# Optimization experiments

Measured on AMD Instinct MI355X. Metric: run time of the kernel, lower is better.

Reference implementation:

```python
import jax, jax.numpy as jnp
import numpy as np

N_NODES = 50000
N_EDGES = 600000
N_RELS = 19
D_IN = 128
D_HID = 64
D_OUT = 2


def setup_inputs() -> dict:
    key = jax.random.key(0)
    ks = jax.random.split(key, 10)
    feat = jax.random.normal(ks[0], (N_NODES, D_IN), dtype=jnp.float32)
    src = jax.random.randint(ks[1], (N_EDGES,), 0, N_NODES)
    dst = jax.random.randint(ks[2], (N_EDGES,), 0, N_NODES)
    etype = jax.random.randint(ks[3], (N_EDGES,), 0, N_RELS)
    s1 = 1.0 / np.sqrt(D_IN)
    s2 = 1.0 / np.sqrt(D_HID)
    W1 = jax.random.normal(ks[4], (N_RELS, D_IN, D_HID), dtype=jnp.float32) * s1
    loop1 = jax.random.normal(ks[5], (D_IN, D_HID), dtype=jnp.float32) * s1
    b1 = jnp.zeros((D_HID,), dtype=jnp.float32)
    W2 = jax.random.normal(ks[6], (N_RELS, D_HID, D_OUT), dtype=jnp.float32) * s2
    loop2 = jax.random.normal(ks[7], (D_HID, D_OUT), dtype=jnp.float32) * s2
    b2 = jnp.zeros((D_OUT,), dtype=jnp.float32)
    return {"feat": feat, "W1": W1, "loop1": loop1, "b1": b1,
            "W2": W2, "loop2": loop2, "b2": b2,
            "src": src, "dst": dst, "etype": etype}


def _rel_graph_conv(h, W, loop_w, bias, src, dst, etype, activation):
    # Per-relation transform of all nodes: [N, R, O]; then gather per edge.
    # (num_rels * out_feat is small, so this is cheaper than gathering W per edge.)
    transformed = jnp.einsum('nd,rdo->nro', h, W)
    msg = transformed[src, etype]                      # [E, O] edge messages
    agg = jax.ops.segment_sum(msg, dst, num_segments=h.shape[0])  # scatter-add
    out = agg + h @ loop_w + bias                      # self-loop + bias
    if activation is not None:
        out = activation(out)
    return out


def reference(feat, W1, loop1, b1, W2, loop2, b2, src, dst, etype):
    h = _rel_graph_conv(feat, W1, loop1, b1, src, dst, etype, jax.nn.relu)
    h = _rel_graph_conv(h, W2, loop2, b2, src, dst, etype, None)
    return h
```

## Files before the change

### kernel.cpp

```cpp
#include <hip/hip_runtime.h>

#define N_NODES 50000
#define N_EDGES 600000
#define N_RELS  19
#define D_IN    128
#define D_HID   64
#define D_OUT   2

typedef unsigned short u16;
typedef unsigned int   u32;
typedef __attribute__((ext_vector_type(8))) short sfrag;
typedef __attribute__((ext_vector_type(4))) float f32x4;

__device__ __forceinline__ u16 f2bf(float f){
  union { float f; u32 i; } v; v.f = f;
  u32 r = v.i + 0x7fffu + ((v.i >> 16) & 1u);
  return (u16)(r >> 16);
}
__device__ __forceinline__ float bf2f(u16 u){
  union { u32 i; float f; } v; v.i = ((u32)u) << 16; return v.f;
}

__global__ void k_prep(const float* __restrict__ W1, const float* __restrict__ loop1,
                       const float* __restrict__ W2,
                       u16* __restrict__ W1Tb, u16* __restrict__ loop1Tb,
                       u16* __restrict__ W2Tb, int* __restrict__ hist_rel,
                       int* __restrict__ hist_dst){
  int idx = blockIdx.x * 256 + threadIdx.x;
  if (idx < N_RELS)  hist_rel[idx] = 0;
  if (idx < N_NODES) hist_dst[idx] = 0;
  const int T1 = N_RELS * D_HID * D_IN;
  const int T2 = T1 + N_RELS * 16 * D_HID;
  const int T3 = T2 + D_HID * D_IN;
  if (idx < T1) {
    int r = idx / (D_HID * D_IN);
    int t = idx - r * (D_HID * D_IN);
    int j = t >> 7, d = t & 127;
    W1Tb[idx] = f2bf(W1[(r * D_IN + d) * D_HID + j]);
  } else if (idx < T2) {
    int k2 = idx - T1;
    int r = k2 / (16 * D_HID);
    int t = k2 - r * (16 * D_HID);
    int n = t >> 6, k = t & 63;
    W2Tb[k2] = (n < D_OUT) ? f2bf(W2[(r * D_HID + k) * D_OUT + n]) : (u16)0;
  } else if (idx < T3) {
    int k2 = idx - T2;
    int j = k2 >> 7, d = k2 & 127;
    loop1Tb[k2] = f2bf(loop1[d * D_HID + j]);
  }
}

__global__ __launch_bounds__(256) void k_fused_pre(const float* __restrict__ feat,
                                                   u16* __restrict__ featb,
                                                   const int* __restrict__ et,
                                                   const int* __restrict__ dst,
                                                   int* __restrict__ hist_rel,
                                                   int* __restrict__ hist_dst){
  int i = blockIdx.x * 256 + threadIdx.x;
  float2 f = ((const float2*)feat)[i];
  ((u32*)featb)[i] = (u32)f2bf(f.x) | ((u32)f2bf(f.y) << 16);
  if (blockIdx.x < (N_EDGES + 255) / 256) {
    __shared__ int lh[N_RELS];
    int tid = threadIdx.x;
    if (tid < N_RELS) lh[tid] = 0;
    __syncthreads();
    int e = blockIdx.x * 256 + tid;
    if (e < N_EDGES) {
      atomicAdd(&lh[et[e]], 1);
      atomicAdd(&hist_dst[dst[e]], 1);
    }
    __syncthreads();
    if (tid < N_RELS && lh[tid]) atomicAdd(&hist_rel[tid], lh[tid]);
  }
}

__global__ void k_scan_rel(const int* __restrict__ hist, int* __restrict__ offs,
                           int* __restrict__ toff, int* __restrict__ cursor){
  if (threadIdx.x == 0) {
    int acc = 0, tacc = 0;
    offs[0] = 0; toff[0] = 0;
    for (int r = 0; r < N_RELS; ++r) {
      cursor[r] = acc;
      int c = hist[r];
      acc += c;                offs[r + 1] = acc;
      tacc += (c + 127) >> 7;  toff[r + 1] = tacc;
    }
  }
}

__global__ __launch_bounds__(256) void k_scan_dst1(const int* __restrict__ hist,
                                                   int* __restrict__ dcsr,
                                                   int* __restrict__ bsum){
  __shared__ int ws[4];
  int tid = threadIdx.x, lane = tid & 63, w = tid >> 6;
  int i = blockIdx.x * 256 + tid;
  int v = (i < N_NODES) ? hist[i] : 0;
  int x = v;
  #pragma unroll
  for (int o = 1; o < 64; o <<= 1) { int u = __shfl_up(x, o); if (lane >= o) x += u; }
  if (lane == 63) ws[w] = x;
  __syncthreads();
  int add = 0;
  for (int j = 0; j < w; ++j) add += ws[j];
  int excl = x - v + add;
  if (i < N_NODES) dcsr[i] = excl;
  if (tid == 255) bsum[blockIdx.x] = excl + v;
}

__global__ __launch_bounds__(256) void k_scan_dst2(int* __restrict__ bsum,
                                                   int* __restrict__ boff){
  __shared__ int ws[4];
  int tid = threadIdx.x, lane = tid & 63, w = tid >> 6;
  int v = (tid < 196) ? bsum[tid] : 0;
  int x = v;
  #pragma unroll
  for (int o = 1; o < 64; o <<= 1) { int u = __shfl_up(x, o); if (lane >= o) x += u; }
  if (lane == 63) ws[w] = x;
  __syncthreads();
  int add = 0;
  for (int j = 0; j < w; ++j) add += ws[j];
  if (tid < 196) boff[tid] = x - v + add;
}

__global__ __launch_bounds__(256) void k_scan_dst3(const int* __restrict__ boff,
                                                   int* __restrict__ dcsr,
                                                   int* __restrict__ cursor){
  int i = blockIdx.x * 256 + threadIdx.x;
  if (i < N_NODES) {
    int val = dcsr[i] + boff[blockIdx.x];
    dcsr[i] = val;
    cursor[i] = val;
  }
  if (i == 0) dcsr[N_NODES] = N_EDGES;
}

__global__ __launch_bounds__(256) void k_scatter_rel(const int* __restrict__ et,
                                                     int* __restrict__ cursor,
                                                     int* __restrict__ perm){
  __shared__ int lh[N_RELS], base[N_RELS];
  int tid = threadIdx.x;
  if (tid < N_RELS) lh[tid] = 0;
  __syncthreads();
  int e = blockIdx.x * 256 + tid;
  int r = 0, my = 0;
  bool valid = e < N_EDGES;
  if (valid) { r = et[e]; my = atomicAdd(&lh[r], 1); }
  __syncthreads();
  if (tid < N_RELS && lh[tid]) base[tid] = atomicAdd(&cursor[tid], lh[tid]);
  __syncthreads();
  if (valid) perm[base[r] + my] = e;
}

__global__ __launch_bounds__(256) void k_selfloop1_mfma(
    const u16* __restrict__ featb, const u16* __restrict__ loop1Tb,
    const float* __restrict__ b1, float* __restrict__ agg1f){
  __shared__ __align__(16) u16 Als[64][136];
  __shared__ __align__(16) u16 Bls[64][136];
  int tid = threadIdx.x;
  int base = blockIdx.x * 64;
  { int j = tid >> 2, seg = tid & 3;
    const uint4* g = (const uint4*)(loop1Tb + j * 128) + seg * 4;
    uint4* d = (uint4*)&Bls[j][seg * 32];
    d[0] = g[0]; d[1] = g[1]; d[2] = g[2]; d[3] = g[3]; }
  { int i = tid >> 2, seg = tid & 3;
    int n = base + i; if (n >= N_NODES) n = N_NODES - 1;
    const uint4* g = (const uint4*)(featb + (size_t)n * D_IN) + seg * 4;
    uint4* d = (uint4*)&Als[i][seg * 32];
    d[0] = g[0]; d[1] = g[1]; d[2] = g[2]; d[3] = g[3]; }
  __syncthreads();

  int w = tid >> 6, lane = tid & 63;
  int r16 = lane & 15, c4 = lane >> 4;
  sfrag aF[4];
  #pragma unroll
  for (int kk = 0; kk < 4; ++kk)
    aF[kk] = *(const sfrag*)&Als[w * 16 + r16][kk * 32 + c4 * 8];
  #pragma unroll
  for (int ct = 0; ct < 4; ++ct) {
    f32x4 acc = {0.f, 0.f, 0.f, 0.f};
    #pragma unroll
    for (int kk = 0; kk < 4; ++kk) {
      sfrag bF = *(const sfrag*)&Bls[ct * 16 + r16][kk * 32 + c4 * 8];
      acc = __builtin_amdgcn_mfma_f32_16x16x32_bf16(aF[kk], bF, acc, 0, 0, 0);
    }
    int col = ct * 16 + r16;
    float bias = b1[col];
    #pragma unroll
    for (int reg = 0; reg < 4; ++reg) {
      int row = base + w * 16 + c4 * 4 + reg;
      if (row < N_NODES) agg1f[(size_t)row * D_HID + col] = acc[reg] + bias;
    }
  }
}

__global__ __launch_bounds__(256) void k_edge1_mfma(
    const u16* __restrict__ featb, const u16* __restrict__ W1Tb,
    const int* __restrict__ src, const int* __restrict__ dst,
    const int* __restrict__ perm, const int* __restrict__ offs,
    const int* __restrict__ toff, const int* __restrict__ dcsr,
    int* __restrict__ cursor, u16* __restrict__ msgbuf){
  __shared__ __align__(16) u16 Als[128][136];
  __shared__ __align__(16) u16 Bls[64][136];
  __shared__ int posIds[128];
  int tid = threadIdx.x, lane = tid & 63, w = tid >> 6;

  int b = blockIdx.x;
  unsigned long long mm = __ballot((lane < N_RELS) && (b >= toff[lane + 1]));
  int rel = __popcll(mm);
  if (rel >= N_RELS) return;
  int ts = offs[rel] + ((b - toff[rel]) << 7);
  int vc = offs[rel + 1] - ts; if (vc > 128) vc = 128;

  {
    int j = tid >> 2, seg = tid & 3;
    const uint4* g = (const uint4*)(W1Tb + ((size_t)rel * 64 + j) * 128) + seg * 4;
    uint4* d = (uint4*)&Bls[j][seg * 32];
    d[0] = g[0]; d[1] = g[1]; d[2] = g[2]; d[3] = g[3];
  }
  #pragma unroll
  for (int p = 0; p < 2; ++p) {
    int i = p * 64 + (tid >> 2), seg = tid & 3;
    if (i < vc) {
      int e = perm[ts + i];
      if (seg == 0) posIds[i] = atomicAdd(&cursor[dst[e]], 1);
      const uint4* g = (const uint4*)(featb + (size_t)src[e] * D_IN) + seg * 4;
      uint4* d = (uint4*)&Als[i][seg * 32];
      d[0] = g[0]; d[1] = g[1]; d[2] = g[2]; d[3] = g[3];
    } else if (seg == 0) posIds[i] = -1;
  }
  __syncthreads();

  int r16 = lane & 15, c4 = lane >> 4;
  sfrag aF[2][4];
  #pragma unroll
  for (int mt = 0; mt < 2; ++mt)
    #pragma unroll
    for (int kk = 0; kk < 4; ++kk)
      aF[mt][kk] = *(const sfrag*)&Als[w * 32 + mt * 16 + r16][kk * 32 + c4 * 8];
  f32x4 accAll[2][4];
  #pragma unroll
  for (int ct = 0; ct < 4; ++ct) {
    sfrag bF[4];
    #pragma unroll
    for (int kk = 0; kk < 4; ++kk)
      bF[kk] = *(const sfrag*)&Bls[ct * 16 + r16][kk * 32 + c4 * 8];
    #pragma unroll
    for (int mt = 0; mt < 2; ++mt) {
      f32x4 acc = {0.f, 0.f, 0.f, 0.f};
      #pragma unroll
      for (int kk = 0; kk < 4; ++kk)
        acc = __builtin_amdgcn_mfma_f32_16x16x32_bf16(aF[mt][kk], bF[kk], acc, 0, 0, 0);
      accAll[mt][ct] = acc;
    }
  }
  float* msg = (float*)&Als[0][0];
  #pragma unroll
  for (int mt = 0; mt < 2; ++mt)
    #pragma unroll
    for (int ct = 0; ct < 4; ++ct) {
      int col = ct * 16 + r16;
      #pragma unroll
      for (int reg = 0; reg < 4; ++reg) {
        int row = w * 32 + mt * 16 + c4 * 4 + reg;
        msg[row * 68 + col] = accAll[mt][ct][reg];
      }
    }
  __syncthreads();
  { int row = tid >> 1, half = tid & 1;
    int pos = posIds[row];
    if (pos >= 0) {
      const float* mr = msg + row * 68 + half * 32;
      u32 pk[16];
      #pragma unroll
      for (int q = 0; q < 16; ++q)
        pk[q] = (u32)f2bf(mr[2 * q]) | ((u32)f2bf(mr[2 * q + 1]) << 16);
      uint4* d = (uint4*)(msgbuf + (size_t)pos * D_HID + half * 32);
      d[0] = *(uint4*)&pk[0];  d[1] = *(uint4*)&pk[4];
      d[2] = *(uint4*)&pk[8];  d[3] = *(uint4*)&pk[12];
    } }
}

__global__ __launch_bounds__(256) void k_agg_relu_self2(
    const u16* __restrict__ msgbuf, const int* __restrict__ dcsr,
    const float* __restrict__ agg1f, const float* __restrict__ loop2,
    const float* __restrict__ b2, u16* __restrict__ h1b,
    float* __restrict__ out){
  int wv = threadIdx.x >> 6, lane = threadIdx.x & 63;
  int n = blockIdx.x * 4 + wv;
  int s = dcsr[n], epos = dcsr[n + 1];
  int h = lane >> 5, c = lane & 31;
  float a0 = 0.f, a1 = 0.f;
  for (int i = s + h; i < epos; i += 2) {
    u32 v = ((const u32*)msgbuf)[(size_t)i * 32 + c];
    a0 += bf2f((u16)(v & 0xffffu));
    a1 += bf2f((u16)(v >> 16));
  }
  a0 += __shfl_down(a0, 32);
  a1 += __shfl_down(a1, 32);
  float p0 = 0.f, p1 = 0.f;
  if (h == 0) {
    float2 sl = ((const float2*)(agg1f + (size_t)n * D_HID))[c];
    float v0 = a0 + sl.x, v1 = a1 + sl.y;
    v0 = v0 > 0.f ? v0 : 0.f;
    v1 = v1 > 0.f ? v1 : 0.f;
    ((u32*)h1b)[(size_t)n * 32 + c] = (u32)f2bf(v0) | ((u32)f2bf(v1) << 16);
    float2 w0 = ((const float2*)loop2)[2 * c];
    float2 w1 = ((const float2*)loop2)[2 * c + 1];
    p0 = v0 * w0.x + v1 * w1.x;
    p1 = v0 * w0.y + v1 * w1.y;
  }
  #pragma unroll
  for (int off = 16; off; off >>= 1) {
    p0 += __shfl_down(p0, off);
    p1 += __shfl_down(p1, off);
  }
  if (lane == 0) {
    out[n * 2]     = p0 + b2[0];
    out[n * 2 + 1] = p1 + b2[1];
  }
}

__global__ __launch_bounds__(256) void k_edge2_mfma(
    const u16* __restrict__ h1b, const u16* __restrict__ W2Tb,
    const int* __restrict__ src, const int* __restrict__ dst,
    const int* __restrict__ perm, const int* __restrict__ offs,
    const int* __restrict__ toff, float* __restrict__ out){
  __shared__ __align__(16) u16 Als[128][72];
  __shared__ __align__(16) u16 Bls[16][72];
  __shared__ int dstIds[128];
  int tid = threadIdx.x, lane = tid & 63, w = tid >> 6;

  int b = blockIdx.x;
  unsigned long long mm = __ballot((lane < N_RELS) && (b >= toff[lane + 1]));
  int rel = __popcll(mm);
  if (rel >= N_RELS) return;
  int ts = offs[rel] + ((b - toff[rel]) << 7);
  int vc = offs[rel + 1] - ts; if (vc > 128) vc = 128;

  if (tid < 128) {
    ((uint4*)&Bls[tid >> 3][0])[tid & 7] = ((const uint4*)(W2Tb + (size_t)rel * 16 * 64))[tid];
  }
  {
    int i = tid >> 1, half = tid & 1;
    if (i < vc) {
      int e = perm[ts + i];
      if (half == 0) dstIds[i] = dst[e];
      const uint4* g = (const uint4*)(h1b + (size_t)src[e] * D_HID) + half * 4;
      uint4* d = (uint4*)&Als[i][half * 32];
      d[0] = g[0]; d[1] = g[1]; d[2] = g[2]; d[3] = g[3];
    } else if (half == 0) dstIds[i] = -1;
  }
  __syncthreads();

  int r16 = lane & 15, c4 = lane >> 4;
  #pragma unroll
  for (int mt = 0; mt < 2; ++mt) {
    f32x4 acc = {0.f, 0.f, 0.f, 0.f};
    #pragma unroll
    for (int kk = 0; kk < 2; ++kk) {
      sfrag aF = *(const sfrag*)&Als[w * 32 + mt * 16 + r16][kk * 32 + c4 * 8];
      sfrag bF = *(const sfrag*)&Bls[r16][kk * 32 + c4 * 8];
      acc = __builtin_amdgcn_mfma_f32_16x16x32_bf16(aF, bF, acc, 0, 0, 0);
    }
    if (r16 < D_OUT) {
      #pragma unroll
      for (int reg = 0; reg < 4; ++reg) {
        int row = w * 32 + mt * 16 + c4 * 4 + reg;
        int dn = dstIds[row];
        if (dn >= 0) atomicAdd(&out[dn * D_OUT + r16], acc[reg]);
      }
    }
  }
}

extern "C" void kernel_launch(void* const* d_in, const int* in_sizes, int n_in,
                              void* d_out, int out_size, void* d_ws, size_t ws_size,
                              hipStream_t stream){
  const float* feat  = (const float*)d_in[0];
  const float* W1    = (const float*)d_in[1];
  const float* loop1 = (const float*)d_in[2];
  const float* b1    = (const float*)d_in[3];
  const float* W2    = (const float*)d_in[4];
  const float* loop2 = (const float*)d_in[5];
  const float* b2    = (const float*)d_in[6];
  const int* src     = (const int*)d_in[7];
  const int* dst     = (const int*)d_in[8];
  const int* et      = (const int*)d_in[9];
  float* out = (float*)d_out;

  char* w = (char*)d_ws;
  u16*   W1Tb     = (u16*)(w);
  u16*   W2Tb     = (u16*)(w + 311296);
  u16*   loop1Tb  = (u16*)(w + 350208);
  int*   hist_rel = (int*)(w + 366592);
  int*   offs     = (int*)(w + 366720);
  int*   toff     = (int*)(w + 366848);
  int*   cur_rel  = (int*)(w + 366976);
  int*   bsum     = (int*)(w + 367104);
  int*   boff     = (int*)(w + 368128);
  int*   hist_dst = (int*)(w + 369152);
  int*   dcsr     = (int*)(w + 569152);
  int*   cur_dst  = (int*)(w + 769168);
  int*   perm     = (int*)(w + 969168);
  u16*   featb    = (u16*)(w + 3369168);
  float* agg1f    = (float*)(w + 16169168);
  u16*   h1b      = (u16*)(w + 28969168);
  u16*   msgbuf   = (u16*)(w + 35369168);

  const int MAX_TILES = (N_EDGES + 127) / 128 + N_RELS;

  k_prep          <<<716,   256, 0, stream>>>(W1, loop1, W2, W1Tb, loop1Tb, W2Tb,
                                              hist_rel, hist_dst);
  k_fused_pre     <<<12500, 256, 0, stream>>>(feat, featb, et, dst, hist_rel, hist_dst);
  k_scan_rel      <<<1,      64, 0, stream>>>(hist_rel, offs, toff, cur_rel);
  k_scan_dst1     <<<196,   256, 0, stream>>>(hist_dst, dcsr, bsum);
  k_scan_dst2     <<<1,     256, 0, stream>>>(bsum, boff);
  k_scan_dst3     <<<196,   256, 0, stream>>>(boff, dcsr, cur_dst);
  k_scatter_rel   <<<2344,  256, 0, stream>>>(et, cur_rel, perm);
  k_selfloop1_mfma<<<(N_NODES + 63) / 64, 256, 0, stream>>>(featb, loop1Tb, b1, agg1f);
  k_edge1_mfma    <<<MAX_TILES, 256, 0, stream>>>(featb, W1Tb, src, dst, perm, offs, toff,
                                                  dcsr, cur_dst, msgbuf);
  k_agg_relu_self2<<<12500, 256, 0, stream>>>(msgbuf, dcsr, agg1f, loop2, b2, h1b, out);
  k_edge2_mfma    <<<MAX_TILES, 256, 0, stream>>>(h1b, W2Tb, src, dst, perm, offs, toff, out);
}
```

Measured before the change: 329.5 us.

## Replace three-pass dst scan with atomic allocation and fuse self-loop into edge kernel

```diff
diff --git a/kernel.cpp b/kernel.cpp
--- a/kernel.cpp
+++ b/kernel.cpp
@@ -6,6 +6,8 @@
 #define D_IN    128
 #define D_HID   64
 #define D_OUT   2
+#define EDGE_TILES ((N_EDGES + 127) / 128 + N_RELS)
+#define SL_BLOCKS  ((N_NODES + 63) / 64)
 
 typedef unsigned short u16;
 typedef unsigned int   u32;
@@ -25,10 +27,11 @@
                        const float* __restrict__ W2,
                        u16* __restrict__ W1Tb, u16* __restrict__ loop1Tb,
                        u16* __restrict__ W2Tb, int* __restrict__ hist_rel,
-                       int* __restrict__ hist_dst){
+                       int* __restrict__ hist_dst, int* __restrict__ gcnt){
   int idx = blockIdx.x * 256 + threadIdx.x;
   if (idx < N_RELS)  hist_rel[idx] = 0;
   if (idx < N_NODES) hist_dst[idx] = 0;
+  if (idx == 0) gcnt[0] = 0;
   const int T1 = N_RELS * D_HID * D_IN;
   const int T2 = T1 + N_RELS * 16 * D_HID;
   const int T3 = T2 + D_HID * D_IN;
@@ -74,64 +77,35 @@
   }
 }
 
-__global__ void k_scan_rel(const int* __restrict__ hist, int* __restrict__ offs,
-                           int* __restrict__ toff, int* __restrict__ cursor){
-  if (threadIdx.x == 0) {
-    int acc = 0, tacc = 0;
-    offs[0] = 0; toff[0] = 0;
-    for (int r = 0; r < N_RELS; ++r) {
-      cursor[r] = acc;
-      int c = hist[r];
-      acc += c;                offs[r + 1] = acc;
-      tacc += (c + 127) >> 7;  toff[r + 1] = tacc;
-    }
-  }
-}
-
-__global__ __launch_bounds__(256) void k_scan_dst1(const int* __restrict__ hist,
-                                                   int* __restrict__ dcsr,
-                                                   int* __restrict__ bsum){
-  __shared__ int ws[4];
-  int tid = threadIdx.x, lane = tid & 63, w = tid >> 6;
-  int i = blockIdx.x * 256 + tid;
-  int v = (i < N_NODES) ? hist[i] : 0;
+__global__ __launch_bounds__(256) void k_alloc_scan(
+    const int* __restrict__ hist_dst, int* __restrict__ dstart,
+    int* __restrict__ cur_dst, int* __restrict__ gcnt,
+    const int* __restrict__ hist_rel, int* __restrict__ offs,
+    int* __restrict__ toff, int* __restrict__ cur_rel){
+  if (blockIdx.x == 196) {
+    if (threadIdx.x == 0) {
+      int acc = 0, tacc = 0;
+      offs[0] = 0; toff[0] = 0;
+      for (int r = 0; r < N_RELS; ++r) {
+        cur_rel[r] = acc;
+        int c = hist_rel[r];
+        acc += c;                offs[r + 1] = acc;
+        tacc += (c + 127) >> 7;  toff[r + 1] = tacc;
+      }
+    }
+    return;
+  }
+  __shared__ int wbase[4];
+  int tid = threadIdx.x, lane = tid & 63, wv = tid >> 6;
+  int n = blockIdx.x * 256 + tid;
+  int v = (n < N_NODES) ? hist_dst[n] : 0;
   int x = v;
   #pragma unroll
   for (int o = 1; o < 64; o <<= 1) { int u = __shfl_up(x, o); if (lane >= o) x += u; }
-  if (lane == 63) ws[w] = x;
-  __syncthreads();
-  int add = 0;
-  for (int j = 0; j < w; ++j) add += ws[j];
-  int excl = x - v + add;
-  if (i < N_NODES) dcsr[i] = excl;
-  if (tid == 255) bsum[blockIdx.x] = excl + v;
-}
-
-__global__ __launch_bounds__(256) void k_scan_dst2(int* __restrict__ bsum,
-                                                   int* __restrict__ boff){
-  __shared__ int ws[4];
-  int tid = threadIdx.x, lane = tid & 63, w = tid >> 6;
-  int v = (tid < 196) ? bsum[tid] : 0;
-  int x = v;
-  #pragma unroll
-  for (int o = 1; o < 64; o <<= 1) { int u = __shfl_up(x, o); if (lane >= o) x += u; }
-  if (lane == 63) ws[w] = x;
-  __syncthreads();
-  int add = 0;
-  for (int j = 0; j < w; ++j) add += ws[j];
-  if (tid < 196) boff[tid] = x - v + add;
-}
-
-__global__ __launch_bounds__(256) void k_scan_dst3(const int* __restrict__ boff,
-                                                   int* __restrict__ dcsr,
-                                                   int* __restrict__ cursor){
-  int i = blockIdx.x * 256 + threadIdx.x;
-  if (i < N_NODES) {
-    int val = dcsr[i] + boff[blockIdx.x];
-    dcsr[i] = val;
-    cursor[i] = val;
-  }
-  if (i == 0) dcsr[N_NODES] = N_EDGES;
+  if (lane == 63) wbase[wv] = atomicAdd(gcnt, x);
+  __syncthreads();
+  int start = wbase[wv] + x - v;
+  if (n < N_NODES) { dstart[n] = start; cur_dst[n] = start; }
 }
 
 __global__ __launch_bounds__(256) void k_scatter_rel(const int* __restrict__ et,
@@ -151,58 +125,48 @@
   if (valid) perm[base[r] + my] = e;
 }
 
-__global__ __launch_bounds__(256) void k_selfloop1_mfma(
-    const u16* __restrict__ featb, const u16* __restrict__ loop1Tb,
-    const float* __restrict__ b1, float* __restrict__ agg1f){
-  __shared__ __align__(16) u16 Als[64][136];
-  __shared__ __align__(16) u16 Bls[64][136];
-  int tid = threadIdx.x;
-  int base = blockIdx.x * 64;
-  { int j = tid >> 2, seg = tid & 3;
-    const uint4* g = (const uint4*)(loop1Tb + j * 128) + seg * 4;
-    uint4* d = (uint4*)&Bls[j][seg * 32];
-    d[0] = g[0]; d[1] = g[1]; d[2] = g[2]; d[3] = g[3]; }
-  { int i = tid >> 2, seg = tid & 3;
-    int n = base + i; if (n >= N_NODES) n = N_NODES - 1;
-    const uint4* g = (const uint4*)(featb + (size_t)n * D_IN) + seg * 4;
-    uint4* d = (uint4*)&Als[i][seg * 32];
-    d[0] = g[0]; d[1] = g[1]; d[2] = g[2]; d[3] = g[3]; }
-  __syncthreads();
-
-  int w = tid >> 6, lane = tid & 63;
-  int r16 = lane & 15, c4 = lane >> 4;
-  sfrag aF[4];
-  #pragma unroll
-  for (int kk = 0; kk < 4; ++kk)
-    aF[kk] = *(const sfrag*)&Als[w * 16 + r16][kk * 32 + c4 * 8];
-  #pragma unroll
-  for (int ct = 0; ct < 4; ++ct) {
-    f32x4 acc = {0.f, 0.f, 0.f, 0.f};
-    #pragma unroll
-    for (int kk = 0; kk < 4; ++kk) {
-      sfrag bF = *(const sfrag*)&Bls[ct * 16 + r16][kk * 32 + c4 * 8];
-      acc = __builtin_amdgcn_mfma_f32_16x16x32_bf16(aF[kk], bF, acc, 0, 0, 0);
-    }
-    int col = ct * 16 + r16;
-    float bias = b1[col];
-    #pragma unroll
-    for (int reg = 0; reg < 4; ++reg) {
-      int row = base + w * 16 + c4 * 4 + reg;
-      if (row < N_NODES) agg1f[(size_t)row * D_HID + col] = acc[reg] + bias;
-    }
-  }
-}
-
-__global__ __launch_bounds__(256) void k_edge1_mfma(
+__global__ __launch_bounds__(256) void k_se1(
     const u16* __restrict__ featb, const u16* __restrict__ W1Tb,
+    const u16* __restrict__ loop1Tb, const float* __restrict__ b1,
     const int* __restrict__ src, const int* __restrict__ dst,
     const int* __restrict__ perm, const int* __restrict__ offs,
-    const int* __restrict__ toff, const int* __restrict__ dcsr,
-    int* __restrict__ cursor, u16* __restrict__ msgbuf){
+    const int* __restrict__ toff, int* __restrict__ cur_dst,
+    u16* __restrict__ msgbuf, float* __restrict__ agg1f){
   __shared__ __align__(16) u16 Als[128][136];
-  __shared__ __align__(16) u16 Bls[64][136];
   __shared__ int posIds[128];
   int tid = threadIdx.x, lane = tid & 63, w = tid >> 6;
+  int r16 = lane & 15, c4 = lane >> 4;
+
+  if (blockIdx.x >= EDGE_TILES) {
+    int base = (blockIdx.x - EDGE_TILES) * 64;
+    { int i = tid >> 2, seg = tid & 3;
+      int n = base + i; if (n >= N_NODES) n = N_NODES - 1;
+      const uint4* g = (const uint4*)(featb + (size_t)n * D_IN) + seg * 4;
+      uint4* d = (uint4*)&Als[i][seg * 32];
+      d[0] = g[0]; d[1] = g[1]; d[2] = g[2]; d[3] = g[3]; }
+    __syncthreads();
+    sfrag aF[4];
+    #pragma unroll
+    for (int kk = 0; kk < 4; ++kk)
+      aF[kk] = *(const sfrag*)&Als[w * 16 + r16][kk * 32 + c4 * 8];
+    #pragma unroll
+    for (int ct = 0; ct < 4; ++ct) {
+      f32x4 acc = {0.f, 0.f, 0.f, 0.f};
+      #pragma unroll
+      for (int kk = 0; kk < 4; ++kk) {
+        sfrag bF = *(const sfrag*)(loop1Tb + ((ct * 16 + r16) << 7) + kk * 32 + c4 * 8);
+        acc = __builtin_amdgcn_mfma_f32_16x16x32_bf16(aF[kk], bF, acc, 0, 0, 0);
+      }
+      int col = ct * 16 + r16;
+      float bias = b1[col];
+      #pragma unroll
+      for (int reg = 0; reg < 4; ++reg) {
+        int row = base + w * 16 + c4 * 4 + reg;
+        if (row < N_NODES) agg1f[(size_t)row * D_HID + col] = acc[reg] + bias;
+      }
+    }
+    return;
+  }
 
   int b = blockIdx.x;
   unsigned long long mm = __ballot((lane < N_RELS) && (b >= toff[lane + 1]));
@@ -211,18 +175,12 @@
   int ts = offs[rel] + ((b - toff[rel]) << 7);
   int vc = offs[rel + 1] - ts; if (vc > 128) vc = 128;
 
-  {
-    int j = tid >> 2, seg = tid & 3;
-    const uint4* g = (const uint4*)(W1Tb + ((size_t)rel * 64 + j) * 128) + seg * 4;
-    uint4* d = (uint4*)&Bls[j][seg * 32];
-    d[0] = g[0]; d[1] = g[1]; d[2] = g[2]; d[3] = g[3];
-  }
   #pragma unroll
   for (int p = 0; p < 2; ++p) {
     int i = p * 64 + (tid >> 2), seg = tid & 3;
     if (i < vc) {
       int e = perm[ts + i];
-      if (seg == 0) posIds[i] = atomicAdd(&cursor[dst[e]], 1);
+      if (seg == 0) posIds[i] = atomicAdd(&cur_dst[dst[e]], 1);
       const uint4* g = (const uint4*)(featb + (size_t)src[e] * D_IN) + seg * 4;
       uint4* d = (uint4*)&Als[i][seg * 32];
       d[0] = g[0]; d[1] = g[1]; d[2] = g[2]; d[3] = g[3];
@@ -230,26 +188,24 @@
   }
   __syncthreads();
 
-  int r16 = lane & 15, c4 = lane >> 4;
   sfrag aF[2][4];
   #pragma unroll
   for (int mt = 0; mt < 2; ++mt)
     #pragma unroll
     for (int kk = 0; kk < 4; ++kk)
       aF[mt][kk] = *(const sfrag*)&Als[w * 32 + mt * 16 + r16][kk * 32 + c4 * 8];
+  const u16* Wr = W1Tb + ((size_t)rel << 13);
   f32x4 accAll[2][4];
   #pragma unroll
   for (int ct = 0; ct < 4; ++ct) {
-    sfrag bF[4];
-    #pragma unroll
-    for (int kk = 0; kk < 4; ++kk)
-      bF[kk] = *(const sfrag*)&Bls[ct * 16 + r16][kk * 32 + c4 * 8];
     #pragma unroll
     for (int mt = 0; mt < 2; ++mt) {
       f32x4 acc = {0.f, 0.f, 0.f, 0.f};
       #pragma unroll
-      for (int kk = 0; kk < 4; ++kk)
-        acc = __builtin_amdgcn_mfma_f32_16x16x32_bf16(aF[mt][kk], bF[kk], acc, 0, 0, 0);
+      for (int kk = 0; kk < 4; ++kk) {
+        sfrag bF = *(const sfrag*)(Wr + ((ct * 16 + r16) << 7) + kk * 32 + c4 * 8);
+        acc = __builtin_amdgcn_mfma_f32_16x16x32_bf16(aF[mt][kk], bF, acc, 0, 0, 0);
+      }
       accAll[mt][ct] = acc;
     }
   }
@@ -281,13 +237,13 @@
 }
 
 __global__ __launch_bounds__(256) void k_agg_relu_self2(
-    const u16* __restrict__ msgbuf, const int* __restrict__ dcsr,
-    const float* __restrict__ agg1f, const float* __restrict__ loop2,
-    const float* __restrict__ b2, u16* __restrict__ h1b,
-    float* __restrict__ out){
+    const u16* __restrict__ msgbuf, const int* __restrict__ dstart,
+    const int* __restrict__ cnt, const float* __restrict__ agg1f,
+    const float* __restrict__ loop2, const float* __restrict__ b2,
+    u16* __restrict__ h1b, float* __restrict__ out){
   int wv = threadIdx.x >> 6, lane = threadIdx.x & 63;
   int n = blockIdx.x * 4 + wv;
-  int s = dcsr[n], epos = dcsr[n + 1];
+  int s = dstart[n], epos = s + cnt[n];
   int h = lane >> 5, c = lane & 31;
   float a0 = 0.f, a1 = 0.f;
   for (int i = s + h; i < epos; i += 2) {
@@ -396,30 +352,26 @@
   int*   offs     = (int*)(w + 366720);
   int*   toff     = (int*)(w + 366848);
   int*   cur_rel  = (int*)(w + 366976);
-  int*   bsum     = (int*)(w + 367104);
-  int*   boff     = (int*)(w + 368128);
-  int*   hist_dst = (int*)(w + 369152);
-  int*   dcsr     = (int*)(w + 569152);
-  int*   cur_dst  = (int*)(w + 769168);
-  int*   perm     = (int*)(w + 969168);
-  u16*   featb    = (u16*)(w + 3369168);
-  float* agg1f    = (float*)(w + 16169168);
-  u16*   h1b      = (u16*)(w + 28969168);
-  u16*   msgbuf   = (u16*)(w + 35369168);
-
-  const int MAX_TILES = (N_EDGES + 127) / 128 + N_RELS;
+  int*   gcnt     = (int*)(w + 367104);
+  int*   hist_dst = (int*)(w + 367232);
+  int*   dstart   = (int*)(w + 567232);
+  int*   cur_dst  = (int*)(w + 767232);
+  int*   perm     = (int*)(w + 967232);
+  u16*   featb    = (u16*)(w + 3367232);
+  float* agg1f    = (float*)(w + 16167232);
+  u16*   h1b      = (u16*)(w + 28967232);
+  u16*   msgbuf   = (u16*)(w + 35367232);
 
   k_prep          <<<716,   256, 0, stream>>>(W1, loop1, W2, W1Tb, loop1Tb, W2Tb,
-                                              hist_rel, hist_dst);
+                                              hist_rel, hist_dst, gcnt);
   k_fused_pre     <<<12500, 256, 0, stream>>>(feat, featb, et, dst, hist_rel, hist_dst);
-  k_scan_rel      <<<1,      64, 0, stream>>>(hist_rel, offs, toff, cur_rel);
-  k_scan_dst1     <<<196,   256, 0, stream>>>(hist_dst, dcsr, bsum);
-  k_scan_dst2     <<<1,     256, 0, stream>>>(bsum, boff);
-  k_scan_dst3     <<<196,   256, 0, stream>>>(boff, dcsr, cur_dst);
+  k_alloc_scan    <<<197,   256, 0, stream>>>(hist_dst, dstart, cur_dst, gcnt,
+                                              hist_rel, offs, toff, cur_rel);
   k_scatter_rel   <<<2344,  256, 0, stream>>>(et, cur_rel, perm);
-  k_selfloop1_mfma<<<(N_NODES + 63) / 64, 256, 0, stream>>>(featb, loop1Tb, b1, agg1f);
-  k_edge1_mfma    <<<MAX_TILES, 256, 0, stream>>>(featb, W1Tb, src, dst, perm, offs, toff,
-                                                  dcsr, cur_dst, msgbuf);
-  k_agg_relu_self2<<<12500, 256, 0, stream>>>(msgbuf, dcsr, agg1f, loop2, b2, h1b, out);
-  k_edge2_mfma    <<<MAX_TILES, 256, 0, stream>>>(h1b, W2Tb, src, dst, perm, offs, toff, out);
-}
+  k_se1           <<<EDGE_TILES + SL_BLOCKS, 256, 0, stream>>>(
+                      featb, W1Tb, loop1Tb, b1, src, dst, perm, offs, toff,
+                      cur_dst, msgbuf, agg1f);
+  k_agg_relu_self2<<<12500, 256, 0, stream>>>(msgbuf, dstart, hist_dst, agg1f,
+                                              loop2, b2, h1b, out);
+  k_edge2_mfma    <<<EDGE_TILES, 256, 0, stream>>>(h1b, W2Tb, src, dst, perm, offs, toff, out);
+}
```

Result: slower. 346.3 us (+5.1%).
